# Performance work log

Measured on AMD Instinct MI355X. Metric: run time of the kernel, lower is better.

The kernel has to match this reference:

```python
import jax, jax.numpy as jnp
import numpy as np

DIN = 128
HID = 128
B, N = 32, 2048
NEG = 9000000000000000.0


def setup_inputs() -> dict:
    key = jax.random.key(0)
    ks = jax.random.split(key, 8)
    x = jax.random.normal(ks[0], (B, N, DIN), dtype=jnp.float32)
    mask = jax.random.randint(ks[1], (B, N, N), 0, 2).astype(jnp.float32)
    s = 1.0 / np.sqrt(DIN)
    Wv = jax.random.uniform(ks[2], (DIN, HID), minval=-s, maxval=s, dtype=jnp.float32)
    bv = jax.random.uniform(ks[3], (HID,), minval=-s, maxval=s, dtype=jnp.float32)
    Wk = jax.random.uniform(ks[4], (DIN, HID), minval=-s, maxval=s, dtype=jnp.float32)
    bk = jax.random.uniform(ks[5], (HID,), minval=-s, maxval=s, dtype=jnp.float32)
    Wq = jax.random.uniform(ks[6], (DIN, HID), minval=-s, maxval=s, dtype=jnp.float32)
    bq = jax.random.uniform(ks[7], (HID,), minval=-s, maxval=s, dtype=jnp.float32)
    return {"x": x, "mask": mask, "Wv": Wv, "bv": bv, "Wk": Wk, "bk": bk, "Wq": Wq, "bq": bq}


def reference(x, mask, Wv, bv, Wk, bk, Wq, bq):
    v = jnp.tanh(x @ Wv + bv)            # [B, N, H]
    q = jnp.tanh(x @ Wq + bq)            # [B, N, H]
    k = jnp.tanh(x @ Wk + bk)            # [B, N, H]
    scores = jnp.einsum('bih,bjh->bij', q, k)  # [B, N, N]
    scores = scores * mask - NEG * (1.0 - mask)
    att = jax.nn.softmax(scores, axis=-1)
    out = jnp.einsum('bij,bjh->bih', att, v)   # [B, N, H]
    return out
```

## Files before the change

### kernel.cpp

```cpp
#include <hip/hip_runtime.h>

#define DIN 128
#define HID 128
#define BB  32
#define NN  2048
#define LOG2E 1.44269504088896340736f

typedef float  f32x4   __attribute__((ext_vector_type(4)));
typedef __bf16 bf16x4v __attribute__((ext_vector_type(4)));
typedef __bf16 bf16x8  __attribute__((ext_vector_type(8)));

__device__ __forceinline__ float tanh_fast(float x) {
  float e = __expf(2.0f * x);
  return 1.0f - 2.0f / (e + 1.0f);
}

__global__ __launch_bounds__(256) void wt_kernel(
    const float* __restrict__ Wq, const float* __restrict__ Wk,
    const float* __restrict__ Wv, __bf16* __restrict__ wt) {
  const float* W = (blockIdx.x == 0) ? Wq : (blockIdx.x == 1) ? Wk : Wv;
  __bf16* dst = wt + blockIdx.x * (DIN * HID);
  int t = threadIdx.x;
#pragma unroll
  for (int c = 0; c < 16; ++c) {
    int o = c * 1024 + t * 4;
    int d = o >> 7, h = o & 127;
    f32x4 v = *(const f32x4*)(W + d * HID + h);
    dst[(h + 0) * DIN + d] = (__bf16)v.x;
    dst[(h + 1) * DIN + d] = (__bf16)v.y;
    dst[(h + 2) * DIN + d] = (__bf16)v.z;
    dst[(h + 3) * DIN + d] = (__bf16)v.w;
  }
}

__global__ __launch_bounds__(256) void proj_kernel(
    const float* __restrict__ x, const __bf16* __restrict__ wt,
    const float* __restrict__ bq, const float* __restrict__ bk,
    const float* __restrict__ bv, __bf16* __restrict__ qbf,
    __bf16* __restrict__ kbf, __bf16* __restrict__ vtbf) {
  int tid = threadIdx.x;
  int lane = tid & 63, w = tid >> 6;
  int l15 = lane & 15, quad = lane >> 4;
  long i0 = (long)blockIdx.x * 64;

  bf16x8 bx[4][4];
#pragma unroll
  for (int nt = 0; nt < 4; ++nt) {
    const float* xp = x + (i0 + nt * 16 + l15) * DIN;
#pragma unroll
    for (int ks = 0; ks < 4; ++ks) {
      int d0 = ks * 32 + quad * 8;
      f32x4 a = *(const f32x4*)(xp + d0);
      f32x4 b = *(const f32x4*)(xp + d0 + 4);
      bf16x8 f;
      f[0] = (__bf16)a.x; f[1] = (__bf16)a.y; f[2] = (__bf16)a.z; f[3] = (__bf16)a.w;
      f[4] = (__bf16)b.x; f[5] = (__bf16)b.y; f[6] = (__bf16)b.z; f[7] = (__bf16)b.w;
      bx[nt][ks] = f;
    }
  }

#pragma unroll
  for (int p = 0; p < 2; ++p) {
    const __bf16* wtp = wt + p * DIN * HID;
    const float* bias = (p == 0) ? bq : bk;
    __bf16* outp = (p == 0) ? qbf : kbf;
#pragma unroll
    for (int nt = 0; nt < 8; ++nt) {
      int h0 = nt * 16 + l15;
      f32x4 acc = {0.f, 0.f, 0.f, 0.f};
#pragma unroll
      for (int ks = 0; ks < 4; ++ks) {
        bf16x8 wf = *(const bf16x8*)(wtp + (long)h0 * DIN + ks * 32 + quad * 8);
        acc = __builtin_amdgcn_mfma_f32_16x16x32_bf16(bx[w][ks], wf, acc, 0, 0, 0);
      }
      float bcol = bias[h0];
      long rowb = i0 + w * 16 + quad * 4;
#pragma unroll
      for (int r = 0; r < 4; ++r) {
        float val = tanh_fast(acc[r] + bcol);
        if (p == 0) val *= LOG2E;
        outp[(rowb + r) * HID + h0] = (__bf16)val;
      }
    }
  }

  {
    const __bf16* wtp = wt + 2 * DIN * HID;
    long bb = i0 >> 11;
    int nloc = (int)(i0 & 2047);
    long vbase = bb * (long)HID * NN;
#pragma unroll
    for (int s = 0; s < 2; ++s) {
      int hb = w * 32 + s * 16;
      bf16x8 af[4];
#pragma unroll
      for (int ks = 0; ks < 4; ++ks)
        af[ks] = *(const bf16x8*)(wtp + (long)(hb + l15) * DIN + ks * 32 + quad * 8);
      float bvr[4];
#pragma unroll
      for (int r = 0; r < 4; ++r) bvr[r] = bv[hb + quad * 4 + r];
#pragma unroll
      for (int nt = 0; nt < 4; ++nt) {
        f32x4 acc = {0.f, 0.f, 0.f, 0.f};
#pragma unroll
        for (int ks = 0; ks < 4; ++ks)
          acc = __builtin_amdgcn_mfma_f32_16x16x32_bf16(af[ks], bx[nt][ks], acc, 0, 0, 0);
        int hrow = hb + quad * 4;
        int ncol = nloc + nt * 16 + l15;
#pragma unroll
        for (int r = 0; r < 4; ++r) {
          float val = tanh_fast(acc[r] + bvr[r]);
          vtbf[vbase + (long)(hrow + r) * NN + ncol] = (__bf16)val;
        }
      }
    }
  }
}

#define KSTR 136
#define VSTR 72
#define PSTR 72

__global__ __launch_bounds__(512, 4) void attn_kernel(
    const __bf16* __restrict__ qbf, const __bf16* __restrict__ kbf,
    const __bf16* __restrict__ vtbf, const float* __restrict__ mask,
    float* __restrict__ out) {
  __shared__ __bf16 Ks[64 * KSTR];
  __shared__ __bf16 Vts[128 * VSTR];
  __shared__ __bf16 Pl[8 * 16 * PSTR];

  const int tid = threadIdx.x;
  const int lane = tid & 63, w = tid >> 6;
  const int l15 = lane & 15, quad = lane >> 4;
  const int bid = blockIdx.x;
  const int vb = (bid >> 3) | ((bid & 7) << 6);
  const int b = vb >> 4;
  const int i0 = (vb & 15) * 128;
  const long kvbase = (long)b * NN * HID;

  bf16x8 qf[4];
  {
    const __bf16* qp = qbf + kvbase + (long)(i0 + w * 16 + l15) * HID + quad * 8;
#pragma unroll
    for (int ks = 0; ks < 4; ++ks) qf[ks] = *(const bf16x8*)(qp + ks * 32);
  }

  const int krow = tid >> 4, kcol = (tid & 15) * 8;
  const int vrow = tid >> 3, vcol = (tid & 7) * 8;
  const __bf16* kg = kbf + kvbase + (long)krow * HID + kcol;
  const __bf16* vg = vtbf + (long)b * HID * NN + (long)vrow * NN + vcol;
  __bf16* ksd0 = Ks + krow * KSTR + kcol;
  __bf16* ksd1 = Ks + (krow + 32) * KSTR + kcol;
  __bf16* vsd0 = Vts + vrow * VSTR + vcol;
  __bf16* vsd1 = Vts + (vrow + 64) * VSTR + vcol;
  const float* mp = mask + ((long)b * NN + (i0 + w * 16 + l15)) * NN + quad * 4;
  __bf16* Pw = Pl + w * 16 * PSTR;

  f32x4 O[8];
#pragma unroll
  for (int i = 0; i < 8; ++i) O[i] = (f32x4){0.f, 0.f, 0.f, 0.f};
  float mrow = -1e30f, lrow = 0.0f;

  bf16x8 kr0 = *(const bf16x8*)(kg);
  bf16x8 kr1 = *(const bf16x8*)(kg + 32 * HID);
  bf16x8 vr0 = *(const bf16x8*)(vg);
  bf16x8 vr1 = *(const bf16x8*)(vg + (long)64 * NN);
  f32x4 mr[4];
#pragma unroll
  for (int t = 0; t < 4; ++t) mr[t] = *(const f32x4*)(mp + t * 16);
  *(bf16x8*)ksd0 = kr0; *(bf16x8*)ksd1 = kr1;
  *(bf16x8*)vsd0 = vr0; *(bf16x8*)vsd1 = vr1;
  unsigned mbits;
  {
    float mb = 0.f;
#pragma unroll
    for (int t = 0; t < 4; ++t)
#pragma unroll
      for (int r = 0; r < 4; ++r)
        mb = fmaf(mr[t][r], (float)(1u << (t * 4 + r)), mb);
    mbits = (unsigned)mb;
  }
  __syncthreads();

  for (int jt = 0; jt < 32; ++jt) {
    const int jn = (jt < 31) ? jt + 1 : 31;
    {
      const __bf16* kgn = kg + (long)jn * 64 * HID;
      kr0 = *(const bf16x8*)(kgn);
      kr1 = *(const bf16x8*)(kgn + 32 * HID);
      const __bf16* vgn = vg + jn * 64;
      vr0 = *(const bf16x8*)(vgn);
      vr1 = *(const bf16x8*)(vgn + (long)64 * NN);
#pragma unroll
      for (int t = 0; t < 4; ++t) mr[t] = *(const f32x4*)(mp + jn * 64 + t * 16);
    }

    f32x4 pt[4];
#pragma unroll
    for (int t = 0; t < 4; ++t) {
      f32x4 acc = {0.f, 0.f, 0.f, 0.f};
      const __bf16* kp = Ks + (t * 16 + l15) * KSTR + quad * 8;
#pragma unroll
      for (int ks = 0; ks < 4; ++ks) {
        bf16x8 kf = *(const bf16x8*)(kp + ks * 32);
        acc = __builtin_amdgcn_mfma_f32_16x16x32_bf16(kf, qf[ks], acc, 0, 0, 0);
      }
      pt[t] = acc;
    }

    float tmx = -1e30f;
#pragma unroll
    for (int t = 0; t < 4; ++t)
#pragma unroll
      for (int r = 0; r < 4; ++r) {
        float s = ((mbits >> (t * 4 + r)) & 1u) ? pt[t][r] : -1e30f;
        pt[t][r] = s;
        tmx = fmaxf(tmx, s);
      }
    tmx = fmaxf(tmx, __shfl_xor(tmx, 16));
    tmx = fmaxf(tmx, __shfl_xor(tmx, 32));
    const float mnew = fmaxf(mrow, tmx);
    const float alpha = exp2f(mrow - mnew);
    float rs = 0.0f;
#pragma unroll
    for (int t = 0; t < 4; ++t)
#pragma unroll
      for (int r = 0; r < 4; ++r) {
        float p = exp2f(pt[t][r] - mnew);
        pt[t][r] = p;
        rs += p;
      }
    rs += __shfl_xor(rs, 16);
    rs += __shfl_xor(rs, 32);
    lrow = lrow * alpha + rs;
    mrow = mnew;

    float ar[4];
#pragma unroll
    for (int r = 0; r < 4; ++r) ar[r] = __shfl(alpha, (quad << 2) + r);
#pragma unroll
    for (int nt = 0; nt < 8; ++nt)
#pragma unroll
      for (int r = 0; r < 4; ++r) O[nt][r] *= ar[r];

#pragma unroll
    for (int t = 0; t < 4; ++t) {
      bf16x4v pb;
#pragma unroll
      for (int r = 0; r < 4; ++r) pb[r] = (__bf16)pt[t][r];
      *(bf16x4v*)(Pw + l15 * PSTR + t * 16 + quad * 4) = pb;
    }
    const bf16x8 pf0 = *(const bf16x8*)(Pw + l15 * PSTR + quad * 8);
    const bf16x8 pf1 = *(const bf16x8*)(Pw + l15 * PSTR + 32 + quad * 8);

#pragma unroll
    for (int nt = 0; nt < 8; ++nt) {
      const __bf16* vp = Vts + (nt * 16 + l15) * VSTR + quad * 8;
      bf16x8 vf0 = *(const bf16x8*)(vp);
      bf16x8 vf1 = *(const bf16x8*)(vp + 32);
      O[nt] = __builtin_amdgcn_mfma_f32_16x16x32_bf16(pf0, vf0, O[nt], 0, 0, 0);
      O[nt] = __builtin_amdgcn_mfma_f32_16x16x32_bf16(pf1, vf1, O[nt], 0, 0, 0);
    }

    __syncthreads();
    *(bf16x8*)ksd0 = kr0; *(bf16x8*)ksd1 = kr1;
    *(bf16x8*)vsd0 = vr0; *(bf16x8*)vsd1 = vr1;
    {
      float mb = 0.f;
#pragma unroll
      for (int t = 0; t < 4; ++t)
#pragma unroll
        for (int r = 0; r < 4; ++r)
          mb = fmaf(mr[t][r], (float)(1u << (t * 4 + r)), mb);
      mbits = (unsigned)mb;
    }
    __syncthreads();
  }

  const float inv = 1.0f / lrow;
  float il[4];
#pragma unroll
  for (int r = 0; r < 4; ++r) il[r] = __shfl(inv, (quad << 2) + r);
  const long rowb = (long)b * NN + i0 + w * 16 + quad * 4;
#pragma unroll
  for (int r = 0; r < 4; ++r) {
    float* op = out + (rowb + r) * HID;
#pragma unroll
    for (int nt = 0; nt < 8; ++nt) op[nt * 16 + l15] = O[nt][r] * il[r];
  }
}

extern "C" void kernel_launch(void* const* d_in, const int* in_sizes, int n_in,
                              void* d_out, int out_size, void* d_ws, size_t ws_size,
                              hipStream_t stream) {
  const float* x    = (const float*)d_in[0];
  const float* mask = (const float*)d_in[1];
  const float* Wv   = (const float*)d_in[2];
  const float* bv   = (const float*)d_in[3];
  const float* Wk   = (const float*)d_in[4];
  const float* bk   = (const float*)d_in[5];
  const float* Wq   = (const float*)d_in[6];
  const float* bq   = (const float*)d_in[7];
  float* out = (float*)d_out;

  __bf16* ws = (__bf16*)d_ws;
  __bf16* wt   = ws;
  __bf16* qbf  = ws + 3 * DIN * HID;
  __bf16* kbf  = qbf + (long)BB * NN * HID;
  __bf16* vtbf = kbf + (long)BB * NN * HID;

  wt_kernel<<<3, 256, 0, stream>>>(Wq, Wk, Wv, wt);
  proj_kernel<<<BB * NN / 64, 256, 0, stream>>>(x, wt, bq, bk, bv, qbf, kbf, vtbf);
  attn_kernel<<<512, 512, 0, stream>>>(qbf, kbf, vtbf, mask, out);
}
```

Measured before the change: 842.9 us.

## Drop LDS staging of K/V and give each wave two query tiles

The attention kernel no longer stages K and V tiles in shared memory with block-wide barriers. Each wave reads its K and V fragments straight from global memory (relying on L1/L2) and handles 32 query rows (two 16-row groups) instead of 16, so each loaded K/V fragment feeds two MFMAs. The block shrinks from 512 to 256 threads, the mask is read with nontemporal loads, and the software prefetch of the next tile is removed. This removes the syncthreads and the LDS copies, but adds redundant global/L2 traffic for K/V across the four waves and raises register pressure from the doubled accumulators.

```diff
diff --git a/kernel.cpp b/kernel.cpp
--- a/kernel.cpp
+++ b/kernel.cpp
@@ -117,17 +117,13 @@
   }
 }
 
-#define KSTR 136
-#define VSTR 72
 #define PSTR 72
 
-__global__ __launch_bounds__(512, 4) void attn_kernel(
+__global__ __launch_bounds__(256) void attn_kernel(
     const __bf16* __restrict__ qbf, const __bf16* __restrict__ kbf,
     const __bf16* __restrict__ vtbf, const float* __restrict__ mask,
     float* __restrict__ out) {
-  __shared__ __bf16 Ks[64 * KSTR];
-  __shared__ __bf16 Vts[128 * VSTR];
-  __shared__ __bf16 Pl[8 * 16 * PSTR];
+  __shared__ __bf16 Pl[4 * 32 * PSTR];
 
   const int tid = threadIdx.x;
   const int lane = tid & 63, w = tid >> 6;
@@ -138,155 +134,138 @@
   const int i0 = (vb & 15) * 128;
   const long kvbase = (long)b * NN * HID;
 
-  bf16x8 qf[4];
-  {
-    const __bf16* qp = qbf + kvbase + (long)(i0 + w * 16 + l15) * HID + quad * 8;
-#pragma unroll
-    for (int ks = 0; ks < 4; ++ks) qf[ks] = *(const bf16x8*)(qp + ks * 32);
-  }
-
-  const int krow = tid >> 4, kcol = (tid & 15) * 8;
-  const int vrow = tid >> 3, vcol = (tid & 7) * 8;
-  const __bf16* kg = kbf + kvbase + (long)krow * HID + kcol;
-  const __bf16* vg = vtbf + (long)b * HID * NN + (long)vrow * NN + vcol;
-  __bf16* ksd0 = Ks + krow * KSTR + kcol;
-  __bf16* ksd1 = Ks + (krow + 32) * KSTR + kcol;
-  __bf16* vsd0 = Vts + vrow * VSTR + vcol;
-  __bf16* vsd1 = Vts + (vrow + 64) * VSTR + vcol;
-  const float* mp = mask + ((long)b * NN + (i0 + w * 16 + l15)) * NN + quad * 4;
-  __bf16* Pw = Pl + w * 16 * PSTR;
-
-  f32x4 O[8];
-#pragma unroll
-  for (int i = 0; i < 8; ++i) O[i] = (f32x4){0.f, 0.f, 0.f, 0.f};
-  float mrow = -1e30f, lrow = 0.0f;
-
-  bf16x8 kr0 = *(const bf16x8*)(kg);
-  bf16x8 kr1 = *(const bf16x8*)(kg + 32 * HID);
-  bf16x8 vr0 = *(const bf16x8*)(vg);
-  bf16x8 vr1 = *(const bf16x8*)(vg + (long)64 * NN);
-  f32x4 mr[4];
-#pragma unroll
-  for (int t = 0; t < 4; ++t) mr[t] = *(const f32x4*)(mp + t * 16);
-  *(bf16x8*)ksd0 = kr0; *(bf16x8*)ksd1 = kr1;
-  *(bf16x8*)vsd0 = vr0; *(bf16x8*)vsd1 = vr1;
-  unsigned mbits;
-  {
-    float mb = 0.f;
-#pragma unroll
-    for (int t = 0; t < 4; ++t)
-#pragma unroll
-      for (int r = 0; r < 4; ++r)
-        mb = fmaf(mr[t][r], (float)(1u << (t * 4 + r)), mb);
-    mbits = (unsigned)mb;
-  }
-  __syncthreads();
-
+  bf16x8 qf[2][4];
+#pragma unroll
+  for (int qg = 0; qg < 2; ++qg) {
+    const __bf16* qp =
+        qbf + kvbase + (long)(i0 + w * 32 + qg * 16 + l15) * HID + quad * 8;
+#pragma unroll
+    for (int ks = 0; ks < 4; ++ks) qf[qg][ks] = *(const bf16x8*)(qp + ks * 32);
+  }
+
+  const __bf16* kgl = kbf + kvbase + (long)l15 * HID + quad * 8;
+  const __bf16* vgl = vtbf + (long)b * HID * NN + (long)l15 * NN + quad * 8;
+  const float* mpl[2];
+#pragma unroll
+  for (int qg = 0; qg < 2; ++qg)
+    mpl[qg] = mask + ((long)b * NN + (i0 + w * 32 + qg * 16 + l15)) * NN + quad * 4;
+  __bf16* Pw = Pl + w * 32 * PSTR;
+
+  f32x4 O[2][8];
+#pragma unroll
+  for (int qg = 0; qg < 2; ++qg)
+#pragma unroll
+    for (int nt = 0; nt < 8; ++nt) O[qg][nt] = (f32x4){0.f, 0.f, 0.f, 0.f};
+  float mrow[2] = {-1e30f, -1e30f}, lrow[2] = {0.0f, 0.0f};
+
+#pragma unroll 1
   for (int jt = 0; jt < 32; ++jt) {
-    const int jn = (jt < 31) ? jt + 1 : 31;
-    {
-      const __bf16* kgn = kg + (long)jn * 64 * HID;
-      kr0 = *(const bf16x8*)(kgn);
-      kr1 = *(const bf16x8*)(kgn + 32 * HID);
-      const __bf16* vgn = vg + jn * 64;
-      vr0 = *(const bf16x8*)(vgn);
-      vr1 = *(const bf16x8*)(vgn + (long)64 * NN);
-#pragma unroll
-      for (int t = 0; t < 4; ++t) mr[t] = *(const f32x4*)(mp + jn * 64 + t * 16);
-    }
-
-    f32x4 pt[4];
+    const int j0 = jt * 64;
+
+    unsigned mbits[2];
+#pragma unroll
+    for (int qg = 0; qg < 2; ++qg) {
+      f32x4 mr[4];
+#pragma unroll
+      for (int t = 0; t < 4; ++t)
+        mr[t] = __builtin_nontemporal_load((const f32x4*)(mpl[qg] + j0 + t * 16));
+      float mb = 0.f;
+#pragma unroll
+      for (int t = 0; t < 4; ++t)
+#pragma unroll
+        for (int r = 0; r < 4; ++r)
+          mb = fmaf(mr[t][r], (float)(1u << (t * 4 + r)), mb);
+      mbits[qg] = (unsigned)mb;
+    }
+
+    f32x4 S[2][4];
 #pragma unroll
     for (int t = 0; t < 4; ++t) {
-      f32x4 acc = {0.f, 0.f, 0.f, 0.f};
-      const __bf16* kp = Ks + (t * 16 + l15) * KSTR + quad * 8;
+      const __bf16* kp = kgl + (long)(j0 + t * 16) * HID;
+      f32x4 a0 = {0.f, 0.f, 0.f, 0.f}, a1 = {0.f, 0.f, 0.f, 0.f};
 #pragma unroll
       for (int ks = 0; ks < 4; ++ks) {
         bf16x8 kf = *(const bf16x8*)(kp + ks * 32);
-        acc = __builtin_amdgcn_mfma_f32_16x16x32_bf16(kf, qf[ks], acc, 0, 0, 0);
-      }
-      pt[t] = acc;
-    }
-
-    float tmx = -1e30f;
-#pragma unroll
-    for (int t = 0; t < 4; ++t)
-#pragma unroll
-      for (int r = 0; r < 4; ++r) {
-        float s = ((mbits >> (t * 4 + r)) & 1u) ? pt[t][r] : -1e30f;
-        pt[t][r] = s;
-        tmx = fmaxf(tmx, s);
-      }
-    tmx = fmaxf(tmx, __shfl_xor(tmx, 16));
-    tmx = fmaxf(tmx, __shfl_xor(tmx, 32));
-    const float mnew = fmaxf(mrow, tmx);
-    const float alpha = exp2f(mrow - mnew);
-    float rs = 0.0f;
-#pragma unroll
-    for (int t = 0; t < 4; ++t)
-#pragma unroll
-      for (int r = 0; r < 4; ++r) {
-        float p = exp2f(pt[t][r] - mnew);
-        pt[t][r] = p;
-        rs += p;
-      }
-    rs += __shfl_xor(rs, 16);
-    rs += __shfl_xor(rs, 32);
-    lrow = lrow * alpha + rs;
-    mrow = mnew;
-
-    float ar[4];
-#pragma unroll
-    for (int r = 0; r < 4; ++r) ar[r] = __shfl(alpha, (quad << 2) + r);
-#pragma unroll
-    for (int nt = 0; nt < 8; ++nt)
-#pragma unroll
-      for (int r = 0; r < 4; ++r) O[nt][r] *= ar[r];
-
-#pragma unroll
-    for (int t = 0; t < 4; ++t) {
-      bf16x4v pb;
-#pragma unroll
-      for (int r = 0; r < 4; ++r) pb[r] = (__bf16)pt[t][r];
-      *(bf16x4v*)(Pw + l15 * PSTR + t * 16 + quad * 4) = pb;
-    }
-    const bf16x8 pf0 = *(const bf16x8*)(Pw + l15 * PSTR + quad * 8);
-    const bf16x8 pf1 = *(const bf16x8*)(Pw + l15 * PSTR + 32 + quad * 8);
+        a0 = __builtin_amdgcn_mfma_f32_16x16x32_bf16(kf, qf[0][ks], a0, 0, 0, 0);
+        a1 = __builtin_amdgcn_mfma_f32_16x16x32_bf16(kf, qf[1][ks], a1, 0, 0, 0);
+      }
+      S[0][t] = a0;
+      S[1][t] = a1;
+    }
+
+#pragma unroll
+    for (int qg = 0; qg < 2; ++qg) {
+      float tmx = -1e30f;
+#pragma unroll
+      for (int t = 0; t < 4; ++t)
+#pragma unroll
+        for (int r = 0; r < 4; ++r) {
+          float s = ((mbits[qg] >> (t * 4 + r)) & 1u) ? S[qg][t][r] : -1e30f;
+          S[qg][t][r] = s;
+          tmx = fmaxf(tmx, s);
+        }
+      tmx = fmaxf(tmx, __shfl_xor(tmx, 16));
+      tmx = fmaxf(tmx, __shfl_xor(tmx, 32));
+      const float mnew = fmaxf(mrow[qg], tmx);
+      const float alpha = exp2f(mrow[qg] - mnew);
+      float rs = 0.0f;
+#pragma unroll
+      for (int t = 0; t < 4; ++t) {
+        bf16x4v pb;
+#pragma unroll
+        for (int r = 0; r < 4; ++r) {
+          float p = exp2f(S[qg][t][r] - mnew);
+          rs += p;
+          pb[r] = (__bf16)p;
+        }
+        *(bf16x4v*)(Pw + (qg * 16 + l15) * PSTR + t * 16 + quad * 4) = pb;
+      }
+      rs += __shfl_xor(rs, 16);
+      rs += __shfl_xor(rs, 32);
+      lrow[qg] = lrow[qg] * alpha + rs;
+      mrow[qg] = mnew;
+      float ar[4];
+#pragma unroll
+      for (int r = 0; r < 4; ++r) ar[r] = __shfl(alpha, (quad << 2) + r);
+#pragma unroll
+      for (int nt = 0; nt < 8; ++nt)
+#pragma unroll
+        for (int r = 0; r < 4; ++r) O[qg][nt][r] *= ar[r];
+    }
+
+    bf16x8 pf[2][2];
+#pragma unroll
+    for (int qg = 0; qg < 2; ++qg)
+#pragma unroll
+      for (int js = 0; js < 2; ++js)
+        pf[qg][js] =
+            *(const bf16x8*)(Pw + (qg * 16 + l15) * PSTR + js * 32 + quad * 8);
 
 #pragma unroll
     for (int nt = 0; nt < 8; ++nt) {
-      const __bf16* vp = Vts + (nt * 16 + l15) * VSTR + quad * 8;
-      bf16x8 vf0 = *(const bf16x8*)(vp);
-      bf16x8 vf1 = *(const bf16x8*)(vp + 32);
-      O[nt] = __builtin_amdgcn_mfma_f32_16x16x32_bf16(pf0, vf0, O[nt], 0, 0, 0);
-      O[nt] = __builtin_amdgcn_mfma_f32_16x16x32_bf16(pf1, vf1, O[nt], 0, 0, 0);
-    }
-
-    __syncthreads();
-    *(bf16x8*)ksd0 = kr0; *(bf16x8*)ksd1 = kr1;
-    *(bf16x8*)vsd0 = vr0; *(bf16x8*)vsd1 = vr1;
-    {
-      float mb = 0.f;
-#pragma unroll
-      for (int t = 0; t < 4; ++t)
-#pragma unroll
-        for (int r = 0; r < 4; ++r)
-          mb = fmaf(mr[t][r], (float)(1u << (t * 4 + r)), mb);
-      mbits = (unsigned)mb;
-    }
-    __syncthreads();
-  }
-
-  const float inv = 1.0f / lrow;
-  float il[4];
-#pragma unroll
-  for (int r = 0; r < 4; ++r) il[r] = __shfl(inv, (quad << 2) + r);
-  const long rowb = (long)b * NN + i0 + w * 16 + quad * 4;
-#pragma unroll
-  for (int r = 0; r < 4; ++r) {
-    float* op = out + (rowb + r) * HID;
-#pragma unroll
-    for (int nt = 0; nt < 8; ++nt) op[nt * 16 + l15] = O[nt][r] * il[r];
+      const __bf16* vp = vgl + (long)(nt * 16) * NN + j0;
+#pragma unroll
+      for (int js = 0; js < 2; ++js) {
+        bf16x8 vf = *(const bf16x8*)(vp + js * 32);
+        O[0][nt] = __builtin_amdgcn_mfma_f32_16x16x32_bf16(pf[0][js], vf, O[0][nt], 0, 0, 0);
+        O[1][nt] = __builtin_amdgcn_mfma_f32_16x16x32_bf16(pf[1][js], vf, O[1][nt], 0, 0, 0);
+      }
+    }
+  }
+
+#pragma unroll
+  for (int qg = 0; qg < 2; ++qg) {
+    const float inv = 1.0f / lrow[qg];
+    float il[4];
+#pragma unroll
+    for (int r = 0; r < 4; ++r) il[r] = __shfl(inv, (quad << 2) + r);
+    const long rowb = (long)b * NN + i0 + w * 32 + qg * 16 + quad * 4;
+#pragma unroll
+    for (int r = 0; r < 4; ++r) {
+      float* op = out + (rowb + r) * HID;
+#pragma unroll
+      for (int nt = 0; nt < 8; ++nt) op[nt * 16 + l15] = O[qg][nt][r] * il[r];
+    }
   }
 }
 
@@ -311,5 +290,5 @@
 
   wt_kernel<<<3, 256, 0, stream>>>(Wq, Wk, Wv, wt);
   proj_kernel<<<BB * NN / 64, 256, 0, stream>>>(x, wt, bq, bk, bv, qbf, kbf, vtbf);
-  attn_kernel<<<512, 512, 0, stream>>>(qbf, kbf, vtbf, mask, out);
-}
+  attn_kernel<<<512, 256, 0, stream>>>(qbf, kbf, vtbf, mask, out);
+}
```

Result: slower. 1.167 ms (+38.4%).

## Precompute mask bitfield in projection kernel and stream compact bits into attention

Applied to the files above, without the earlier changes.

Extra blocks are appended to the projection kernel. They read the fp32 mask once and pack each 16-element group into a 16-bit bitfield in workspace. The attention kernel then loads one ushort per tile instead of four float4 mask loads, which cuts in-loop global traffic and register pressure. The P tile is now written to LDS inside the exp loop, and the main loop is kept rolled. The full mask still has to be read once, but that read now runs in a separate, fully parallel pass.

```diff
diff --git a/kernel.cpp b/kernel.cpp
--- a/kernel.cpp
+++ b/kernel.cpp
@@ -5,6 +5,8 @@
 #define BB  32
 #define NN  2048
 #define LOG2E 1.44269504088896340736f
+#define PROJ_BLOCKS 1024
+#define COMP_BLOCKS 32768
 
 typedef float  f32x4   __attribute__((ext_vector_type(4)));
 typedef __bf16 bf16x4v __attribute__((ext_vector_type(4)));
@@ -36,9 +38,29 @@
 __global__ __launch_bounds__(256) void proj_kernel(
     const float* __restrict__ x, const __bf16* __restrict__ wt,
     const float* __restrict__ bq, const float* __restrict__ bk,
-    const float* __restrict__ bv, __bf16* __restrict__ qbf,
-    __bf16* __restrict__ kbf, __bf16* __restrict__ vtbf) {
-  int tid = threadIdx.x;
+    const float* __restrict__ bv, const float* __restrict__ mask,
+    __bf16* __restrict__ qbf, __bf16* __restrict__ kbf,
+    __bf16* __restrict__ vtbf, unsigned short* __restrict__ bits) {
+  const int tid = threadIdx.x;
+
+  if (blockIdx.x >= PROJ_BLOCKS) {
+    const long cidx = (long)(blockIdx.x - PROJ_BLOCKS) * 256 + tid;
+    const int quad = (int)(cidx & 3);
+    const int jt = (int)((cidx >> 2) & 31);
+    const long grow = cidx >> 7;
+    const float* mp = mask + grow * NN + jt * 64 + quad * 4;
+    float mb = 0.f;
+#pragma unroll
+    for (int t = 0; t < 4; ++t) {
+      f32x4 mr = *(const f32x4*)(mp + t * 16);
+#pragma unroll
+      for (int r = 0; r < 4; ++r)
+        mb = fmaf(mr[r], (float)(1u << (t * 4 + r)), mb);
+    }
+    bits[cidx] = (unsigned short)(unsigned)mb;
+    return;
+  }
+
   int lane = tid & 63, w = tid >> 6;
   int l15 = lane & 15, quad = lane >> 4;
   long i0 = (long)blockIdx.x * 64;
@@ -123,7 +145,7 @@
 
 __global__ __launch_bounds__(512, 4) void attn_kernel(
     const __bf16* __restrict__ qbf, const __bf16* __restrict__ kbf,
-    const __bf16* __restrict__ vtbf, const float* __restrict__ mask,
+    const __bf16* __restrict__ vtbf, const unsigned short* __restrict__ bits,
     float* __restrict__ out) {
   __shared__ __bf16 Ks[64 * KSTR];
   __shared__ __bf16 Vts[128 * VSTR];
@@ -140,7 +162,8 @@
 
   bf16x8 qf[4];
   {
-    const __bf16* qp = qbf + kvbase + (long)(i0 + w * 16 + l15) * HID + quad * 8;
+    const __bf16* qp =
+        qbf + kvbase + (long)(i0 + w * 16 + l15) * HID + quad * 8;
 #pragma unroll
     for (int ks = 0; ks < 4; ++ks) qf[ks] = *(const bf16x8*)(qp + ks * 32);
   }
@@ -153,7 +176,8 @@
   __bf16* ksd1 = Ks + (krow + 32) * KSTR + kcol;
   __bf16* vsd0 = Vts + vrow * VSTR + vcol;
   __bf16* vsd1 = Vts + (vrow + 64) * VSTR + vcol;
-  const float* mp = mask + ((long)b * NN + (i0 + w * 16 + l15)) * NN + quad * 4;
+  const unsigned short* bitp =
+      bits + ((long)b * NN + (i0 + w * 16 + l15)) * 128 + quad;
   __bf16* Pw = Pl + w * 16 * PSTR;
 
   f32x4 O[8];
@@ -165,23 +189,12 @@
   bf16x8 kr1 = *(const bf16x8*)(kg + 32 * HID);
   bf16x8 vr0 = *(const bf16x8*)(vg);
   bf16x8 vr1 = *(const bf16x8*)(vg + (long)64 * NN);
-  f32x4 mr[4];
-#pragma unroll
-  for (int t = 0; t < 4; ++t) mr[t] = *(const f32x4*)(mp + t * 16);
+  unsigned mcur = bitp[0];
   *(bf16x8*)ksd0 = kr0; *(bf16x8*)ksd1 = kr1;
   *(bf16x8*)vsd0 = vr0; *(bf16x8*)vsd1 = vr1;
-  unsigned mbits;
-  {
-    float mb = 0.f;
-#pragma unroll
-    for (int t = 0; t < 4; ++t)
-#pragma unroll
-      for (int r = 0; r < 4; ++r)
-        mb = fmaf(mr[t][r], (float)(1u << (t * 4 + r)), mb);
-    mbits = (unsigned)mb;
-  }
   __syncthreads();
 
+#pragma unroll 1
   for (int jt = 0; jt < 32; ++jt) {
     const int jn = (jt < 31) ? jt + 1 : 31;
     {
@@ -191,11 +204,10 @@
       const __bf16* vgn = vg + jn * 64;
       vr0 = *(const bf16x8*)(vgn);
       vr1 = *(const bf16x8*)(vgn + (long)64 * NN);
-#pragma unroll
-      for (int t = 0; t < 4; ++t) mr[t] = *(const f32x4*)(mp + jn * 64 + t * 16);
-    }
-
-    f32x4 pt[4];
+    }
+    const unsigned mnext = bitp[jn * 4];
+
+    f32x4 S[4];
 #pragma unroll
     for (int t = 0; t < 4; ++t) {
       f32x4 acc = {0.f, 0.f, 0.f, 0.f};
@@ -205,7 +217,7 @@
         bf16x8 kf = *(const bf16x8*)(kp + ks * 32);
         acc = __builtin_amdgcn_mfma_f32_16x16x32_bf16(kf, qf[ks], acc, 0, 0, 0);
       }
-      pt[t] = acc;
+      S[t] = acc;
     }
 
     float tmx = -1e30f;
@@ -213,8 +225,8 @@
     for (int t = 0; t < 4; ++t)
 #pragma unroll
       for (int r = 0; r < 4; ++r) {
-        float s = ((mbits >> (t * 4 + r)) & 1u) ? pt[t][r] : -1e30f;
-        pt[t][r] = s;
+        float s = ((mcur >> (t * 4 + r)) & 1u) ? S[t][r] : -1e30f;
+        S[t][r] = s;
         tmx = fmaxf(tmx, s);
       }
     tmx = fmaxf(tmx, __shfl_xor(tmx, 16));
@@ -223,13 +235,16 @@
     const float alpha = exp2f(mrow - mnew);
     float rs = 0.0f;
 #pragma unroll
-    for (int t = 0; t < 4; ++t)
+    for (int t = 0; t < 4; ++t) {
+      bf16x4v pb;
 #pragma unroll
       for (int r = 0; r < 4; ++r) {
-        float p = exp2f(pt[t][r] - mnew);
-        pt[t][r] = p;
+        float p = exp2f(S[t][r] - mnew);
         rs += p;
-      }
+        pb[r] = (__bf16)p;
+      }
+      *(bf16x4v*)(Pw + l15 * PSTR + t * 16 + quad * 4) = pb;
+    }
     rs += __shfl_xor(rs, 16);
     rs += __shfl_xor(rs, 32);
     lrow = lrow * alpha + rs;
@@ -243,13 +258,6 @@
 #pragma unroll
       for (int r = 0; r < 4; ++r) O[nt][r] *= ar[r];
 
-#pragma unroll
-    for (int t = 0; t < 4; ++t) {
-      bf16x4v pb;
-#pragma unroll
-      for (int r = 0; r < 4; ++r) pb[r] = (__bf16)pt[t][r];
-      *(bf16x4v*)(Pw + l15 * PSTR + t * 16 + quad * 4) = pb;
-    }
     const bf16x8 pf0 = *(const bf16x8*)(Pw + l15 * PSTR + quad * 8);
     const bf16x8 pf1 = *(const bf16x8*)(Pw + l15 * PSTR + 32 + quad * 8);
 
@@ -265,15 +273,7 @@
     __syncthreads();
     *(bf16x8*)ksd0 = kr0; *(bf16x8*)ksd1 = kr1;
     *(bf16x8*)vsd0 = vr0; *(bf16x8*)vsd1 = vr1;
-    {
-      float mb = 0.f;
-#pragma unroll
-      for (int t = 0; t < 4; ++t)
-#pragma unroll
-        for (int r = 0; r < 4; ++r)
-          mb = fmaf(mr[t][r], (float)(1u << (t * 4 + r)), mb);
-      mbits = (unsigned)mb;
-    }
+    mcur = mnext;
     __syncthreads();
   }
 
@@ -308,8 +308,10 @@
   __bf16* qbf  = ws + 3 * DIN * HID;
   __bf16* kbf  = qbf + (long)BB * NN * HID;
   __bf16* vtbf = kbf + (long)BB * NN * HID;
+  unsigned short* bits = (unsigned short*)(vtbf + (long)BB * NN * HID);
 
   wt_kernel<<<3, 256, 0, stream>>>(Wq, Wk, Wv, wt);
-  proj_kernel<<<BB * NN / 64, 256, 0, stream>>>(x, wt, bq, bk, bv, qbf, kbf, vtbf);
-  attn_kernel<<<512, 512, 0, stream>>>(qbf, kbf, vtbf, mask, out);
-}
+  proj_kernel<<<PROJ_BLOCKS + COMP_BLOCKS, 256, 0, stream>>>(
+      x, wt, bq, bk, bv, mask, qbf, kbf, vtbf, bits);
+  attn_kernel<<<512, 512, 0, stream>>>(qbf, kbf, vtbf, bits, out);
+}
```

Result: slower. 912.9 us (+8.3%).
